# Optimization experiments

Measured on AMD Instinct MI355X. Metric: run time of the kernel, lower is better.

## Reference

```python
import jax, jax.numpy as jnp
import numpy as np
import math

B, S, D, H, R = 4, 4096, 1024, 16, 256
DK = D // H

def setup_inputs() -> dict:
    key = jax.random.key(0)
    ks = jax.random.split(key, 16)
    def lin(k, fan_in, fan_out):
        # torch Linear default init: U(-1/sqrt(fan_in), 1/sqrt(fan_in))
        bound = 1.0 / math.sqrt(fan_in)
        kw, kb = jax.random.split(k)
        W = jax.random.uniform(kw, (fan_out, fan_in), jnp.float32, -bound, bound)
        b = jax.random.uniform(kb, (fan_out,), jnp.float32, -bound, bound)
        return W, b
    Wq, bq = lin(ks[0], D, D)
    Wk, bk = lin(ks[1], D, D)
    Wv, bv = lin(ks[2], D, D)
    Wo, bo = lin(ks[3], D, D)
    # xavier_uniform over last two dims (S, R)
    xav = math.sqrt(6.0 / (S + R))
    E = jax.random.uniform(ks[4], (H, S, R), jnp.float32, -xav, xav)
    F = jax.random.uniform(ks[5], (H, S, R), jnp.float32, -xav, xav)
    query = jax.random.normal(ks[6], (B, S, D), jnp.float32)
    key_ = jax.random.normal(ks[7], (B, S, D), jnp.float32)
    value = jax.random.normal(ks[8], (B, S, D), jnp.float32)
    return {"query": query, "key": key_, "value": value,
            "Wq": Wq, "bq": bq, "Wk": Wk, "bk": bk, "Wv": Wv, "bv": bv,
            "Wo": Wo, "bo": bo, "E": E, "F": F}

def _split_heads(x):
    # [B, S, D] -> [B, H, S, DK]
    b, s, _ = x.shape
    return x.reshape(b, s, H, DK).transpose(0, 2, 1, 3)

def reference(query, key, value, Wq, bq, Wk, bk, Wv, bv, Wo, bo, E, F):
    q = _split_heads(query @ Wq.T + bq)   # [B,H,S,DK]
    k = _split_heads(key @ Wk.T + bk)
    v = _split_heads(value @ Wv.T + bv)
    # key^T @ E : [B,H,DK,S] @ [H,S,R] -> [B,H,DK,R]
    kp = jnp.einsum('bhsd,hsr->bhdr', k, E)
    vp = jnp.einsum('bhsd,hsr->bhdr', v, F)
    attn = jnp.einsum('bhsd,bhdr->bhsr', q, kp) / math.sqrt(DK)
    attn = jax.nn.softmax(attn, axis=-1)  # [B,H,S,R]
    out = jnp.einsum('bhsr,bhdr->bhsd', attn, vp)  # [B,H,S,DK]
    out = out.transpose(0, 2, 1, 3).reshape(query.shape[0], -1, D)
    return out @ Wo.T + bo
```

## Files before the change

kernel.cpp:

```cpp
#include <hip/hip_runtime.h>


typedef __bf16 bf16;
typedef bf16 bf16x8 __attribute__((ext_vector_type(8)));
typedef bf16 bf16x4 __attribute__((ext_vector_type(4)));
typedef float f32x4 __attribute__((ext_vector_type(4)));

constexpr int BB = 4, SS = 4096, DD = 1024, HH = 16, RR = 256, DK = 64;

#define QSCALE 0.1803368801111204f

__device__ __forceinline__ void gl2lds16(const void* g, void* l, int lane)
{
#if __has_builtin(__builtin_amdgcn_global_load_lds)
    auto gp = reinterpret_cast<const __attribute__((address_space(1))) void*>(
        reinterpret_cast<uintptr_t>(g));
    auto lp = reinterpret_cast<__attribute__((address_space(3))) void*>(
        reinterpret_cast<uintptr_t>(l));
    __builtin_amdgcn_global_load_lds(gp, lp, 16, 0, 0);
    (void)lane;
#else
    *(bf16x8*)((char*)l + lane * 16) = *(const bf16x8*)g;
#endif
}

__global__ void cvt_f32_bf16(const float* __restrict__ in, bf16* __restrict__ out, int n)
{
    int i = (blockIdx.x * 256 + threadIdx.x) * 8;
    if (i < n) {
        float4 v0 = *(const float4*)(in + i);
        float4 v1 = *(const float4*)(in + i + 4);
        bf16x8 h;
        h[0] = (bf16)v0.x; h[1] = (bf16)v0.y; h[2] = (bf16)v0.z; h[3] = (bf16)v0.w;
        h[4] = (bf16)v1.x; h[5] = (bf16)v1.y; h[6] = (bf16)v1.z; h[7] = (bf16)v1.w;
        *(bf16x8*)(out + i) = h;
    }
}

__global__ void transpose_cvt(const float* __restrict__ in, bf16* __restrict__ out,
                              int rows, int cols)
{
    __shared__ float t[64][65];
    const float* I = in + (size_t)blockIdx.z * rows * cols;
    bf16* O = out + (size_t)blockIdx.z * rows * cols;
    int c0 = blockIdx.x * 64, r0 = blockIdx.y * 64;
    int tx = threadIdx.x, ty = threadIdx.y;
#pragma unroll
    for (int i = ty; i < 64; i += 4)
        t[i][tx] = I[(size_t)(r0 + i) * cols + c0 + tx];
    __syncthreads();
#pragma unroll
    for (int i = ty; i < 64; i += 4)
        O[(size_t)(c0 + i) * rows + r0 + tx] = (bf16)t[tx][i];
}

template <bool OUT_F32>
__global__ __launch_bounds__(512, 2) void gemm_bt(const bf16* __restrict__ A,
                                                  const bf16* __restrict__ W,
                                                  const float* __restrict__ bias,
                                                  void* __restrict__ Cp,
                                                  int M, int N, int K, float oscale)
{
    __shared__ bf16 As[2][256][64];
    __shared__ bf16 Bs[2][256][64];
    const int tid = threadIdx.x, wv = tid >> 6, lane = tid & 63;
    const int g = lane >> 4, lr = lane & 15;

    const int nwg = gridDim.x;
    const int cpx = nwg >> 3;
    const int bid = blockIdx.x;
    const int swz = (bid & 7) * cpx + (bid >> 3);
    const int gx = N >> 8;
    const int mt = swz / gx, nt = swz % gx;
    const int m0 = mt * 256, n0 = nt * 256;
    const int wm = (wv >> 2) * 128, wn = (wv & 3) * 64;

    const int srow = wv * 8 + (lane >> 3);
    const int scol = (lane & 7) * 8;

    f32x4 acc[8][4] = {};

    auto STAGE = [&](int pb, int kt) {
        const int k0 = kt * 64;
#pragma unroll
        for (int j = 0; j < 4; ++j) {
            gl2lds16(A + (size_t)(m0 + j * 64 + srow) * K + k0 + scol,
                     &As[pb][j * 64 + wv * 8][0], lane);
            gl2lds16(W + (size_t)(n0 + j * 64 + srow) * K + k0 + scol,
                     &Bs[pb][j * 64 + wv * 8][0], lane);
        }
    };

    auto COMPUTE = [&](int pb) {
#pragma unroll
        for (int kk = 0; kk < 2; ++kk) {
            bf16x8 b[4];
#pragma unroll
            for (int n = 0; n < 4; ++n)
                b[n] = *(const bf16x8*)&Bs[pb][wn + n * 16 + lr][kk * 32 + g * 8];
#pragma unroll
            for (int m = 0; m < 8; ++m) {
                bf16x8 a = *(const bf16x8*)&As[pb][wm + m * 16 + lr][kk * 32 + g * 8];
#pragma unroll
                for (int n = 0; n < 4; ++n)
                    acc[m][n] = __builtin_amdgcn_mfma_f32_16x16x32_bf16(a, b[n], acc[m][n], 0, 0, 0);
            }
        }
    };

    const int ntk = K >> 6;
    STAGE(0, 0);
    __syncthreads();
    int pb = 0;
    for (int t = 0; t < ntk - 1; ++t) {
        STAGE(pb ^ 1, t + 1);
        COMPUTE(pb);
        __syncthreads();
        pb ^= 1;
    }
    COMPUTE(pb);

#pragma unroll
    for (int n = 0; n < 4; ++n) {
        int col = n0 + wn + n * 16 + lr;
        float bv = bias[col];
#pragma unroll
        for (int m = 0; m < 8; ++m) {
            int row = m0 + wm + m * 16 + 4 * g;
#pragma unroll
            for (int i = 0; i < 4; ++i) {
                float v = (acc[m][n][i] + bv) * oscale;
                if constexpr (OUT_F32)
                    ((float*)Cp)[(size_t)(row + i) * N + col] = v;
                else
                    ((bf16*)Cp)[(size_t)(row + i) * N + col] = (bf16)v;
            }
        }
    }
}

__global__ __launch_bounds__(256) void kpvp_gemm(const bf16* __restrict__ X,
                                                 const bf16* __restrict__ P,
                                                 float* __restrict__ out)
{
    __shared__ bf16 Ak[64][40];
    __shared__ bf16 Bs[256][32];
    const int b = blockIdx.z, h = blockIdx.y;
    const int s0 = blockIdx.x * 512;
    const int tid = threadIdx.x, wv = tid >> 6, lane = tid & 63;
    const int g = lane >> 4, lr = lane & 15;
    const int lrow = lane >> 2, lcol = (lane & 3) * 8;
    const bf16* Pg = P + ((size_t)h * RR + wv * 64 + lrow) * SS + lcol;
    f32x4 acc[4][4] = {};

    for (int kt = 0; kt < 512; kt += 32) {
        const int sb = s0 + kt;
        __syncthreads();
#pragma unroll
        for (int j = 0; j < 4; ++j)
            gl2lds16(Pg + (size_t)(j * 16) * SS + sb, &Bs[wv * 64 + j * 16][0], lane);
        {
            int sl = tid >> 3, dblk = (tid & 7) * 8;
            bf16x8 v = *(const bf16x8*)(X + ((size_t)b * SS + sb + sl) * DD + h * DK + dblk);
#pragma unroll
            for (int j = 0; j < 8; ++j) Ak[dblk + j][sl] = v[j];
        }
        __syncthreads();

        bf16x8 a[4], bb[4];
#pragma unroll
        for (int m = 0; m < 4; ++m) a[m] = *(const bf16x8*)&Ak[m * 16 + lr][g * 8];
#pragma unroll
        for (int n = 0; n < 4; ++n) bb[n] = *(const bf16x8*)&Bs[wv * 64 + n * 16 + lr][g * 8];
#pragma unroll
        for (int m = 0; m < 4; ++m)
#pragma unroll
            for (int n = 0; n < 4; ++n)
                acc[m][n] = __builtin_amdgcn_mfma_f32_16x16x32_bf16(a[m], bb[n], acc[m][n], 0, 0, 0);
    }

    float* o = out + ((size_t)(b * HH + h)) * DK * RR;
#pragma unroll
    for (int m = 0; m < 4; ++m)
#pragma unroll
        for (int n = 0; n < 4; ++n) {
            int r = wv * 64 + n * 16 + lr;
#pragma unroll
            for (int i = 0; i < 4; ++i)
                atomicAdd(o + (size_t)(m * 16 + 4 * g + i) * RR + r, acc[m][n][i]);
        }
}

__global__ __launch_bounds__(512) void attn_fused(const bf16* __restrict__ qb,
                                                  const bf16* __restrict__ kpt,
                                                  const bf16* __restrict__ vpb,
                                                  bf16* __restrict__ ctx)
{
    __shared__ bf16 KPs[256][72];
    __shared__ bf16 VPs[64][264];
    __shared__ bf16 Ps[8][16][264];
    const int b = blockIdx.z, h = blockIdx.y, qt = blockIdx.x;
    const int tid = threadIdx.x, wv = tid >> 6, lane = tid & 63;
    const int g = lane >> 4, lr = lane & 15;
    const bf16* kph = kpt + ((size_t)(b * HH + h)) * RR * DK;
    const bf16* vph = vpb + ((size_t)(b * HH + h)) * DK * RR;

#pragma unroll
    for (int p = 0; p < 4; ++p) {
        int f = p * 512 + tid;
        *(bf16x8*)&KPs[f >> 3][(f & 7) * 8] = *(const bf16x8*)(kph + (size_t)f * 8);
        *(bf16x8*)&VPs[f >> 5][(f & 31) * 8] = *(const bf16x8*)(vph + (size_t)f * 8);
    }

    const bf16* qbase = qb + (size_t)b * SS * DD + h * DK;
    int row0 = qt * 1024 + wv * 16;
    bf16x8 aq0 = *(const bf16x8*)(qbase + (size_t)(row0 + lr) * DD + g * 8);
    bf16x8 aq1 = *(const bf16x8*)(qbase + (size_t)(row0 + lr) * DD + 32 + g * 8);
    __syncthreads();

    for (int it = 0; it < 8; ++it) {
        f32x4 acc[16] = {};
        __builtin_amdgcn_s_setprio(1);
#pragma unroll
        for (int nf = 0; nf < 16; ++nf) {
            bf16x8 b0 = *(const bf16x8*)&KPs[nf * 16 + lr][g * 8];
            bf16x8 b1 = *(const bf16x8*)&KPs[nf * 16 + lr][32 + g * 8];
            acc[nf] = __builtin_amdgcn_mfma_f32_16x16x32_bf16(aq0, b0, acc[nf], 0, 0, 0);
            acc[nf] = __builtin_amdgcn_mfma_f32_16x16x32_bf16(aq1, b1, acc[nf], 0, 0, 0);
        }
        __builtin_amdgcn_s_setprio(0);

        bf16x8 aqn0 = aq0, aqn1 = aq1;
        if (it < 7) {
            const bf16* qr = qbase + (size_t)(row0 + 128 + lr) * DD;
            aqn0 = *(const bf16x8*)(qr + g * 8);
            aqn1 = *(const bf16x8*)(qr + 32 + g * 8);
        }

        float rs[4];
#pragma unroll
        for (int i = 0; i < 4; ++i) {
            float s = 0.f;
#pragma unroll
            for (int nf = 0; nf < 16; ++nf) {
                float pv = exp2f(acc[nf][i]);
                acc[nf][i] = pv;
                s += pv;
            }
#pragma unroll
            for (int msk = 1; msk < 16; msk <<= 1) s += __shfl_xor(s, msk, 64);
            rs[i] = 1.f / s;
        }

#pragma unroll
        for (int nf = 0; nf < 16; ++nf)
#pragma unroll
            for (int i = 0; i < 4; ++i)
                Ps[wv][4 * g + i][nf * 16 + lr] = (bf16)acc[nf][i];
        __builtin_amdgcn_wave_barrier();

        f32x4 o[4] = {};
        __builtin_amdgcn_s_setprio(1);
#pragma unroll
        for (int ks = 0; ks < 8; ++ks) {
            bf16x8 pa = *(const bf16x8*)&Ps[wv][lr][ks * 32 + g * 8];
#pragma unroll
            for (int n = 0; n < 4; ++n) {
                bf16x8 vb = *(const bf16x8*)&VPs[n * 16 + lr][ks * 32 + g * 8];
                o[n] = __builtin_amdgcn_mfma_f32_16x16x32_bf16(pa, vb, o[n], 0, 0, 0);
            }
        }
        __builtin_amdgcn_s_setprio(0);
        __builtin_amdgcn_wave_barrier();

#pragma unroll
        for (int n = 0; n < 4; ++n)
#pragma unroll
            for (int i = 0; i < 4; ++i)
                Ps[wv][4 * g + i][n * 16 + lr] = (bf16)(o[n][i] * rs[i]);
        __builtin_amdgcn_wave_barrier();
        bf16* crow = ctx + (size_t)(b * SS + row0) * DD + h * DK;
#pragma unroll
        for (int p = 0; p < 2; ++p) {
            int r = p * 8 + (lane >> 3), c = (lane & 7) * 8;
            bf16x8 ov = *(const bf16x8*)&Ps[wv][r][c];
            *(bf16x8*)(crow + (size_t)r * DD + c) = ov;
        }
        __builtin_amdgcn_wave_barrier();

        aq0 = aqn0; aq1 = aqn1;
        row0 += 128;
    }
}

extern "C" void kernel_launch(void* const* d_in, const int* in_sizes, int n_in,
                              void* d_out, int out_size, void* d_ws, size_t ws_size,
                              hipStream_t stream)
{
    const float* query = (const float*)d_in[0];
    const float* key   = (const float*)d_in[1];
    const float* value = (const float*)d_in[2];
    const float* Wq = (const float*)d_in[3];  const float* bq = (const float*)d_in[4];
    const float* Wk = (const float*)d_in[5];  const float* bk = (const float*)d_in[6];
    const float* Wv = (const float*)d_in[7];  const float* bv = (const float*)d_in[8];
    const float* Wo = (const float*)d_in[9];  const float* bo = (const float*)d_in[10];
    const float* E  = (const float*)d_in[11];
    const float* F  = (const float*)d_in[12];

    char* w = (char*)d_ws;
    size_t off = 0;
    auto alloc = [&](size_t bytes) -> char* {
        char* p = w + off;
        off += (bytes + 255) & ~(size_t)255;
        return p;
    };

    const size_t DW   = (size_t)DD * DD;
    const size_t BSD  = (size_t)BB * SS * DD;
    const size_t HRS  = (size_t)HH * RR * SS;
    const size_t BHDR = (size_t)BB * HH * DK * RR;

    bf16* wqb = (bf16*)alloc(DW * 2);
    bf16* wkb = (bf16*)alloc(DW * 2);
    bf16* wvb = (bf16*)alloc(DW * 2);
    bf16* wob = (bf16*)alloc(DW * 2);
    bf16* ebt = (bf16*)alloc(HRS * 2);
    bf16* fbt = (bf16*)alloc(HRS * 2);
    bf16* qin = (bf16*)alloc(BSD * 2);
    bf16* kin = (bf16*)alloc(BSD * 2);
    bf16* vin = (bf16*)alloc(BSD * 2);
    bf16* qbuf = (bf16*)alloc(BSD * 2);
    bf16* kbuf = (bf16*)alloc(BSD * 2);
    bf16* vbuf = (bf16*)alloc(BSD * 2);
    if (off > ws_size) return;

    float* kpf  = (float*)qin;
    float* vpf  = kpf + BHDR;
    bf16*  kpt  = (bf16*)kin;
    bf16*  vpbb = kpt + BHDR;
    bf16*  ctx  = (bf16*)vin;

    cvt_f32_bf16<<<(int)(DW / 2048), 256, 0, stream>>>(Wq, wqb, (int)DW);
    cvt_f32_bf16<<<(int)(DW / 2048), 256, 0, stream>>>(Wk, wkb, (int)DW);
    cvt_f32_bf16<<<(int)(DW / 2048), 256, 0, stream>>>(Wv, wvb, (int)DW);
    cvt_f32_bf16<<<(int)(DW / 2048), 256, 0, stream>>>(Wo, wob, (int)DW);
    cvt_f32_bf16<<<(int)(BSD / 2048), 256, 0, stream>>>(query, qin, (int)BSD);
    cvt_f32_bf16<<<(int)(BSD / 2048), 256, 0, stream>>>(key,   kin, (int)BSD);
    cvt_f32_bf16<<<(int)(BSD / 2048), 256, 0, stream>>>(value, vin, (int)BSD);

    dim3 tb(64, 4);
    transpose_cvt<<<dim3(RR / 64, SS / 64, HH), tb, 0, stream>>>(E, ebt, SS, RR);
    transpose_cvt<<<dim3(RR / 64, SS / 64, HH), tb, 0, stream>>>(F, fbt, SS, RR);

    const int nwg = ((BB * SS) / 256) * (DD / 256);
    gemm_bt<false><<<nwg, 512, 0, stream>>>(qin, wqb, bq, qbuf, BB * SS, DD, DD, QSCALE);
    gemm_bt<false><<<nwg, 512, 0, stream>>>(kin, wkb, bk, kbuf, BB * SS, DD, DD, 1.0f);
    gemm_bt<false><<<nwg, 512, 0, stream>>>(vin, wvb, bv, vbuf, BB * SS, DD, DD, 1.0f);

    hipMemsetAsync(kpf, 0, BHDR * 4 * 2, stream);
    kpvp_gemm<<<dim3(SS / 512, HH, BB), 256, 0, stream>>>(kbuf, ebt, kpf);
    kpvp_gemm<<<dim3(SS / 512, HH, BB), 256, 0, stream>>>(vbuf, fbt, vpf);

    transpose_cvt<<<dim3(RR / 64, DK / 64, BB * HH), tb, 0, stream>>>(kpf, kpt, DK, RR);
    cvt_f32_bf16<<<(int)(BHDR / 2048), 256, 0, stream>>>(vpf, vpbb, (int)BHDR);

    attn_fused<<<dim3(SS / 1024, HH, BB), 512, 0, stream>>>(qbuf, kpt, vpbb, ctx);

    gemm_bt<true><<<nwg, 512, 0, stream>>>(ctx, wob, bo, d_out, BB * SS, DD, DD, 1.0f);
}
```

Before: 462.5 us.

## Restructure projection GEMM into 8-phase pipelined schedule with swizzled LDS

```diff
diff --git a/kernel.cpp b/kernel.cpp
--- a/kernel.cpp
+++ b/kernel.cpp
@@ -24,6 +24,10 @@
 #endif
 }
 
+#define VMW4  asm volatile("s_waitcnt vmcnt(4)" ::: "memory")
+#define VMW0  asm volatile("s_waitcnt vmcnt(0)" ::: "memory")
+#define LGKM0 asm volatile("s_waitcnt lgkmcnt(0)" ::: "memory")
+
 __global__ void cvt_f32_bf16(const float* __restrict__ in, bf16* __restrict__ out, int n)
 {
     int i = (blockIdx.x * 256 + threadIdx.x) * 8;
@@ -75,66 +79,121 @@
     const int m0 = mt * 256, n0 = nt * 256;
     const int wm = (wv >> 2) * 128, wn = (wv & 3) * 64;
 
-    const int srow = wv * 8 + (lane >> 3);
-    const int scol = (lane & 7) * 8;
+    const int lrow8 = lane >> 3;
+    const int gcol = ((lane & 7) ^ lrow8) * 8;
 
     f32x4 acc[8][4] = {};
 
-    auto STAGE = [&](int pb, int kt) {
-        const int k0 = kt * 64;
-#pragma unroll
-        for (int j = 0; j < 4; ++j) {
-            gl2lds16(A + (size_t)(m0 + j * 64 + srow) * K + k0 + scol,
-                     &As[pb][j * 64 + wv * 8][0], lane);
-            gl2lds16(W + (size_t)(n0 + j * 64 + srow) * K + k0 + scol,
-                     &Bs[pb][j * 64 + wv * 8][0], lane);
+    auto stageA = [&](int buf, int tk, int h) {
+#pragma unroll
+        for (int s2 = 0; s2 < 2; ++s2) {
+            int j = wv + s2 * 8;
+            int rb = h * 64 + (j >> 3) * 128 + (j & 7) * 8;
+            gl2lds16(A + (size_t)(m0 + rb + lrow8) * 1024 + tk * 64 + gcol,
+                     &As[buf][rb][0], lane);
         }
     };
-
-    auto COMPUTE = [&](int pb) {
-#pragma unroll
-        for (int kk = 0; kk < 2; ++kk) {
-            bf16x8 b[4];
-#pragma unroll
-            for (int n = 0; n < 4; ++n)
-                b[n] = *(const bf16x8*)&Bs[pb][wn + n * 16 + lr][kk * 32 + g * 8];
+    auto stageB = [&](int buf, int tk, int h) {
+#pragma unroll
+        for (int s2 = 0; s2 < 2; ++s2) {
+            int j = wv + s2 * 8;
+            int rb = h * 32 + (j >> 2) * 64 + (j & 3) * 8;
+            gl2lds16(W + (size_t)(n0 + rb + lrow8) * 1024 + tk * 64 + gcol,
+                     &Bs[buf][rb][0], lane);
+        }
+    };
+
+#define PHASE(PB, MH, NH, STAGE_STMT, VM_STMT)                                   \
+    {                                                                            \
+        bf16x8 aF[4][2], bF[2][2];                                               \
+        _Pragma("unroll") for (int m = 0; m < 4; ++m) {                          \
+            _Pragma("unroll") for (int kk = 0; kk < 2; ++kk) {                   \
+                aF[m][kk] = *(const bf16x8*)((const char*)&As[PB][wm + MH * 64 + m * 16 + lr][0] \
+                              + (((kk * 4 + g) ^ (lr & 7)) << 4)); } }           \
+        _Pragma("unroll") for (int n = 0; n < 2; ++n) {                          \
+            _Pragma("unroll") for (int kk = 0; kk < 2; ++kk) {                   \
+                bF[n][kk] = *(const bf16x8*)((const char*)&Bs[PB][wn + NH * 32 + n * 16 + lr][0] \
+                              + (((kk * 4 + g) ^ (lr & 7)) << 4)); } }           \
+        STAGE_STMT;                                                              \
+        VM_STMT;                                                                 \
+        __builtin_amdgcn_s_barrier();                                            \
+        LGKM0;                                                                   \
+        __builtin_amdgcn_sched_barrier(0);                                       \
+        __builtin_amdgcn_s_setprio(1);                                           \
+        _Pragma("unroll") for (int kk = 0; kk < 2; ++kk) {                       \
+            _Pragma("unroll") for (int m = 0; m < 4; ++m) {                      \
+                _Pragma("unroll") for (int n = 0; n < 2; ++n) {                  \
+                    acc[MH * 4 + m][NH * 2 + n] = __builtin_amdgcn_mfma_f32_16x16x32_bf16( \
+                        aF[m][kk], bF[n][kk], acc[MH * 4 + m][NH * 2 + n], 0, 0, 0); } } } \
+        __builtin_amdgcn_s_setprio(0);                                           \
+        __builtin_amdgcn_s_barrier();                                            \
+    }
+
+    stageA(0, 0, 0); stageB(0, 0, 0); stageA(0, 0, 1); stageB(0, 0, 1);
+    stageA(1, 1, 0); stageB(1, 1, 0);
+    VMW4;
+    __builtin_amdgcn_s_barrier();
+
+#pragma unroll 1
+    for (int t = 0; t < 14; t += 2) {
+        PHASE(0, 0, 0, stageA(1, t + 1, 1), (void)0);
+        PHASE(0, 0, 1, stageB(1, t + 1, 1), (void)0);
+        PHASE(0, 1, 0, stageA(0, t + 2, 0), (void)0);
+        PHASE(0, 1, 1, stageB(0, t + 2, 0), VMW4);
+        PHASE(1, 0, 0, stageA(0, t + 2, 1), (void)0);
+        PHASE(1, 0, 1, stageB(0, t + 2, 1), (void)0);
+        PHASE(1, 1, 0, stageA(1, t + 3, 0), (void)0);
+        PHASE(1, 1, 1, stageB(1, t + 3, 0), VMW4);
+    }
+    PHASE(0, 0, 0, stageA(1, 15, 1), (void)0);
+    PHASE(0, 0, 1, stageB(1, 15, 1), (void)0);
+    PHASE(0, 1, 0, (void)0, (void)0);
+    PHASE(0, 1, 1, (void)0, VMW0);
+    PHASE(1, 0, 0, (void)0, (void)0);
+    PHASE(1, 0, 1, (void)0, (void)0);
+    PHASE(1, 1, 0, (void)0, (void)0);
+    PHASE(1, 1, 1, (void)0, (void)0);
+#undef PHASE
+
+    float bv[4];
+#pragma unroll
+    for (int n = 0; n < 4; ++n) bv[n] = bias[n0 + wn + n * 16 + lr];
+
+    if constexpr (OUT_F32) {
+#pragma unroll
+        for (int n = 0; n < 4; ++n) {
+            int col = n0 + wn + n * 16 + lr;
 #pragma unroll
             for (int m = 0; m < 8; ++m) {
-                bf16x8 a = *(const bf16x8*)&As[pb][wm + m * 16 + lr][kk * 32 + g * 8];
-#pragma unroll
-                for (int n = 0; n < 4; ++n)
-                    acc[m][n] = __builtin_amdgcn_mfma_f32_16x16x32_bf16(a, b[n], acc[m][n], 0, 0, 0);
+                int row = m0 + wm + m * 16 + 4 * g;
+#pragma unroll
+                for (int i = 0; i < 4; ++i)
+                    ((float*)Cp)[(size_t)(row + i) * N + col] = (acc[m][n][i] + bv[n]) * oscale;
             }
         }
-    };
-
-    const int ntk = K >> 6;
-    STAGE(0, 0);
-    __syncthreads();
-    int pb = 0;
-    for (int t = 0; t < ntk - 1; ++t) {
-        STAGE(pb ^ 1, t + 1);
-        COMPUTE(pb);
-        __syncthreads();
-        pb ^= 1;
-    }
-    COMPUTE(pb);
-
-#pragma unroll
-    for (int n = 0; n < 4; ++n) {
-        int col = n0 + wn + n * 16 + lr;
-        float bv = bias[col];
-#pragma unroll
-        for (int m = 0; m < 8; ++m) {
-            int row = m0 + wm + m * 16 + 4 * g;
-#pragma unroll
-            for (int i = 0; i < 4; ++i) {
-                float v = (acc[m][n][i] + bv) * oscale;
-                if constexpr (OUT_F32)
-                    ((float*)Cp)[(size_t)(row + i) * N + col] = v;
-                else
-                    ((bf16*)Cp)[(size_t)(row + i) * N + col] = (bf16)v;
+    } else {
+        bf16* myb = (wv < 4) ? (&As[0][0][0] + wv * 8192)
+                             : (&Bs[0][0][0] + (wv - 4) * 8192);
+#pragma unroll
+        for (int m = 0; m < 8; ++m)
+#pragma unroll
+            for (int n = 0; n < 4; ++n) {
+                int colb = n * 32 + lr * 2;
+#pragma unroll
+                for (int i = 0; i < 4; ++i) {
+                    int row = m * 16 + 4 * g + i;
+                    *(bf16*)((char*)myb + row * 128 + (colb ^ ((row & 7) << 4))) =
+                        (bf16)((acc[m][n][i] + bv[n]) * oscale);
+                }
             }
+        __builtin_amdgcn_wave_barrier();
+        bf16* Cb = (bf16*)Cp + (size_t)(m0 + wm) * N + n0 + wn;
+#pragma unroll
+        for (int it = 0; it < 16; ++it) {
+            int r = it * 8 + lrow8;
+            int sl = lane & 7;
+            bf16x8 vv = *(const bf16x8*)((const char*)myb + r * 128 + ((sl ^ (r & 7)) << 4));
+            *(bf16x8*)(Cb + (size_t)r * N + sl * 8) = vv;
         }
     }
 }
```

New measurement: 434.8 us. -6.0%, faster.
